# Kernel tuning notes

Hardware: AMD Instinct MI355X
Metric: run time of the kernel (lower is better)

Reference implementation:

```python
import jax, jax.numpy as jnp
import numpy as np

N_EMBD = 512
N_EXPERTS = 4
TOP_K = 2
D_FF = 4 * N_EMBD


def setup_inputs() -> dict:
    key = jax.random.key(0)
    k_x, k_g, k_w1, k_w2 = jax.random.split(key, 4)
    b, t = 8, 2048
    x = jax.random.normal(k_x, (b, t, N_EMBD), dtype=jnp.float32)
    # Linear layers are bias-free; kaiming-uniform-ish init scale
    gate_w = jax.random.normal(k_g, (N_EMBD, N_EXPERTS), dtype=jnp.float32) * (1.0 / np.sqrt(N_EMBD))
    w1 = jax.random.normal(k_w1, (N_EXPERTS, N_EMBD, D_FF), dtype=jnp.float32) * (1.0 / np.sqrt(N_EMBD))
    w2 = jax.random.normal(k_w2, (N_EXPERTS, D_FF, N_EMBD), dtype=jnp.float32) * (1.0 / np.sqrt(D_FF))
    return {"x": x, "gate_w": gate_w, "w1": w1, "w2": w2}


def reference(x, gate_w, w1, w2):
    # Eval mode: UnitCenteredNoise and Dropout are identity.
    b, t, c = x.shape
    xf = x.reshape(b * t, c)                         # [N, C]
    n = xf.shape[0]

    gate_logits = xf @ gate_w                        # [N, E]
    gate_probs = jax.nn.softmax(gate_logits, axis=-1)
    top_w, top_i = jax.lax.top_k(gate_probs, TOP_K)  # [N, K]
    top_w = top_w / jnp.clip(jnp.sum(top_w, axis=-1, keepdims=True), 1e-6)

    # Sparse router weights [N, E]: zeros except normalized top-k probs.
    router_sparse = jnp.zeros((n, N_EXPERTS), dtype=top_w.dtype)
    router_sparse = router_sparse.at[jnp.arange(n)[:, None], top_i].set(top_w)

    # Per-expert MLP on all tokens, combined with the sparse router weights.
    # Mathematically identical to the masked dispatch/combine in the original.
    h = jnp.einsum('nc,ech->enh', xf, w1)            # [E, N, 4C]
    h = jax.nn.gelu(h, approximate=False)            # torch F.gelu default = erf
    y = jnp.einsum('enh,ehc->enc', h, w2)            # [E, N, C]
    out_flat = jnp.einsum('ne,enc->nc', router_sparse, y)

    return out_flat.reshape(b, t, c), router_sparse
```

## Files before the change

kernel.cpp:

```cpp
#include <hip/hip_runtime.h>
#include <hip/hip_fp16.h>


#define NTOK  16384
#define CDIM  512
#define FF    2048
#define NEXP  4
#define CAP   33280
#define NBLK  260
#define BM    128
#define BN1   128
#define BN2   128
#define BK    32
#define CPAD  32

typedef _Float16 f16;
typedef __attribute__((ext_vector_type(8))) _Float16 f16x8;
typedef __attribute__((ext_vector_type(4))) _Float16 f16x4;
typedef __attribute__((ext_vector_type(4))) float f32x4;

__device__ __forceinline__ void gload16(const void* g, void* l) {
  __builtin_amdgcn_global_load_lds(
      (const __attribute__((address_space(1))) unsigned int*)g,
      (__attribute__((address_space(3))) unsigned int*)l, 16, 0, 0);
}

__device__ __forceinline__ float gelu_fast(float v) {
  float az = fabsf(v) * 0.7071067811865476f;
  float t = __builtin_amdgcn_rcpf(fmaf(0.3275911f, az, 1.0f));
  float p = fmaf(fmaf(fmaf(fmaf(1.061405429f, t, -1.453152027f), t,
                           1.421413741f), t, -0.284496736f), t, 0.254829592f) * t;
  float e = __builtin_amdgcn_exp2f(az * az * -1.4426950408889634f);
  float erfa = fmaf(-p, e, 1.0f);
  float u = copysignf(erfa, v);
  return 0.5f * v * (1.0f + u);
}

__device__ __forceinline__ int xcd_swz(int bid, int nwg) {
  int q = nwg >> 3, r = nwg & 7;
  int x = bid & 7, o = bid >> 3;
  return (x < r ? x * (q + 1) : r * (q + 1) + (x - r) * q) + o;
}


__global__ __launch_bounds__(256) void k_init(int* list, int* cnt) {
  int i = blockIdx.x * 256 + threadIdx.x;
  if (i < CAP) list[i] = -1;
  if (i < 4) cnt[i * CPAD] = 0;
}

__global__ __launch_bounds__(256) void k_cast_t(const float* __restrict__ in,
                                                f16* __restrict__ out, int R, int Cc) {
  __shared__ f16 T[64][72];
  int ez = blockIdx.z;
  const float* ine = in + (size_t)ez * R * Cc;
  f16* oute = out + (size_t)ez * R * Cc;
  int c0 = blockIdx.x * 64;
  int r0 = blockIdx.y * 64;
  int t = threadIdx.x;
  {
    int rr = t >> 2, cc = (t & 3) * 16;
    const float* src = ine + (size_t)(r0 + rr) * Cc + c0 + cc;
    union { f16 h[16]; uint4 u[2]; } pk;
#pragma unroll
    for (int j = 0; j < 16; j += 4) {
      float4 a = *(const float4*)(src + j);
      pk.h[j] = (f16)a.x; pk.h[j + 1] = (f16)a.y;
      pk.h[j + 2] = (f16)a.z; pk.h[j + 3] = (f16)a.w;
    }
    *(uint4*)&T[rr][cc] = pk.u[0];
    *(uint4*)&T[rr][cc + 8] = pk.u[1];
  }
  __syncthreads();
  {
    int oc = t >> 2, orr = (t & 3) * 16;
    union { f16 h[16]; uint4 u[2]; } pk;
#pragma unroll
    for (int j = 0; j < 16; ++j) pk.h[j] = T[orr + j][oc];
    f16* dst = oute + (size_t)(c0 + oc) * R + r0 + orr;
    *(uint4*)dst = pk.u[0];
    *(uint4*)(dst + 8) = pk.u[1];
  }
}


__global__ __launch_bounds__(256) void k_router(const float* __restrict__ x,
                                                const float* __restrict__ gw,
                                                f16* __restrict__ xh,
                                                float* __restrict__ rout,
                                                float4* __restrict__ tokinfo,
                                                int* __restrict__ cnt) {
  __shared__ int lcnt[4];
  int tid = threadIdx.x;
  if (tid < 4) lcnt[tid] = 0;
  __syncthreads();
  int wv = tid >> 6, lane = tid & 63;
  const float4* g = ((const float4*)gw) + lane * 8;
  float4 gv[8];
#pragma unroll
  for (int j = 0; j < 8; ++j) gv[j] = g[j];

  int tok0 = blockIdx.x * 64 + wv * 16;
  for (int i = 0; i < 16; ++i) {
    int tok = tok0 + i;
    const float4* xr = (const float4*)(x + (size_t)tok * CDIM + lane * 8);
    float4 a0 = xr[0], a1 = xr[1];
    union { f16 h[8]; uint4 u; } pk;
    pk.h[0] = (f16)a0.x; pk.h[1] = (f16)a0.y; pk.h[2] = (f16)a0.z; pk.h[3] = (f16)a0.w;
    pk.h[4] = (f16)a1.x; pk.h[5] = (f16)a1.y; pk.h[6] = (f16)a1.z; pk.h[7] = (f16)a1.w;
    *(uint4*)(xh + (size_t)tok * CDIM + lane * 8) = pk.u;
    float xv[8] = {a0.x, a0.y, a0.z, a0.w, a1.x, a1.y, a1.z, a1.w};
    float l0 = 0, l1 = 0, l2 = 0, l3 = 0;
#pragma unroll
    for (int j = 0; j < 8; ++j) {
      float4 g4 = gv[j];
      l0 = fmaf(xv[j], g4.x, l0); l1 = fmaf(xv[j], g4.y, l1);
      l2 = fmaf(xv[j], g4.z, l2); l3 = fmaf(xv[j], g4.w, l3);
    }
#pragma unroll
    for (int off = 32; off; off >>= 1) {
      l0 += __shfl_xor(l0, off); l1 += __shfl_xor(l1, off);
      l2 += __shfl_xor(l2, off); l3 += __shfl_xor(l3, off);
    }
    if (lane == 0) {
      float lg[4] = {l0, l1, l2, l3};
      float m = fmaxf(fmaxf(lg[0], lg[1]), fmaxf(lg[2], lg[3]));
      float p[4], s = 0.f;
#pragma unroll
      for (int e = 0; e < 4; ++e) { p[e] = expf(lg[e] - m); s += p[e]; }
      int i0 = 0;
#pragma unroll
      for (int e = 1; e < 4; ++e) if (lg[e] > lg[i0]) i0 = e;
      int i1 = -1;
#pragma unroll
      for (int e = 0; e < 4; ++e)
        if (e != i0 && (i1 < 0 || lg[e] > lg[i1])) i1 = e;
      float p0 = p[i0] / s, p1 = p[i1] / s;
      float ss = fmaxf(p0 + p1, 1e-6f);
      float w0 = p0 / ss, w1v = p1 / ss;
      float r[4] = {0.f, 0.f, 0.f, 0.f};
      r[i0] = w0; r[i1] = w1v;
      *(float4*)(rout + tok * 4) = make_float4(r[0], r[1], r[2], r[3]);
      float4 ti;
      ti.x = __int_as_float(i0); ti.y = __int_as_float(i1); ti.z = w0; ti.w = w1v;
      tokinfo[tok] = ti;
      atomicAdd(&lcnt[i0], 1);
      atomicAdd(&lcnt[i1], 1);
    }
  }
  __syncthreads();
  if (tid < 4) atomicAdd(cnt + tid * CPAD, lcnt[tid]);
}

__global__ void k_bases(const int* __restrict__ cnt, int* __restrict__ base,
                        int* __restrict__ cursor) {
  if (threadIdx.x == 0 && blockIdx.x == 0) {
    int b = 0;
#pragma unroll
    for (int e = 0; e < 4; ++e) {
      base[e] = b; cursor[e * CPAD] = b;
      b += (cnt[e * CPAD] + 127) & ~127;
    }
    base[4] = b;
  }
}

__global__ __launch_bounds__(256) void k_assign(const float4* __restrict__ tokinfo,
                                                int* cursor, int* __restrict__ list,
                                                int2* __restrict__ tokslot) {
  __shared__ int lcnt[4], lbase[4];
  int tid = threadIdx.x;
  if (tid < 4) lcnt[tid] = 0;
  __syncthreads();
  int t0 = blockIdx.x * 1024 + tid * 4;
  float4 ti[4]; int lo0[4], lo1[4];
#pragma unroll
  for (int j = 0; j < 4; ++j) {
    ti[j] = tokinfo[t0 + j];
    lo0[j] = atomicAdd(&lcnt[__float_as_int(ti[j].x)], 1);
    lo1[j] = atomicAdd(&lcnt[__float_as_int(ti[j].y)], 1);
  }
  __syncthreads();
  if (tid < 4) lbase[tid] = atomicAdd(cursor + tid * CPAD, lcnt[tid]);
  __syncthreads();
#pragma unroll
  for (int j = 0; j < 4; ++j) {
    int s0 = lbase[__float_as_int(ti[j].x)] + lo0[j];
    list[s0] = t0 + j;
    int s1 = lbase[__float_as_int(ti[j].y)] + lo1[j];
    list[s1] = t0 + j;
    tokslot[t0 + j] = make_int2(s0, s1);
  }
}


__global__ __launch_bounds__(256, 4) void k_gemm1(const f16* __restrict__ xh,
                                                  const f16* __restrict__ w1t,
                                                  const int* __restrict__ list,
                                                  const int* __restrict__ base,
                                                  f16* __restrict__ H, int cb, int nwg) {
  __shared__ __align__(16) char smem[32768 + 512];
  int* slist = (int*)(smem + 32768);
  int tid = threadIdx.x;
  int wk = xcd_swz(blockIdx.x, nwg);
  int bx = wk >> 4, by = wk & 15;
  int m0 = (cb + bx) * BM;
  int mloc = bx * BM;
  int h0 = by * BN1;
  int e = 0;
#pragma unroll
  for (int i = 1; i < 4; ++i) if (m0 >= base[i]) e = i;
  if (tid < BM) {
    int v = list[m0 + tid];
    slist[tid] = v < 0 ? 0 : v;
  }
  __syncthreads();

  int tokr[2];
#pragma unroll
  for (int i = 0; i < 2; ++i) tokr[i] = slist[i * 64 + (tid >> 2)];

  const f16* wB = w1t + (size_t)(e * FF + h0) * CDIM;
  int kbs = ((tid & 3) * 16) ^ (((tid >> 3) & 3) << 4);

  f32x4 acc[4][4] = {};
  int lane = tid & 63, w = tid >> 6, wr = w >> 1, wc = w & 1;

  auto stage = [&](int kk, int p) {
    char* s = smem + p * 16384;
#pragma unroll
    for (int i = 0; i < 2; ++i) {
      gload16(xh + (size_t)tokr[i] * CDIM + kk * BK + (kbs >> 1),
              s + i * 4096 + tid * 16);
    }
#pragma unroll
    for (int i = 0; i < 2; ++i) {
      int row = i * 64 + (tid >> 2);
      gload16(wB + (size_t)row * CDIM + kk * BK + (kbs >> 1),
              s + 8192 + i * 4096 + tid * 16);
    }
  };

  auto compute = [&](int p) {
    const char* s = smem + p * 16384;
    f16x8 af[4], bfr[4];
    int kb = (lane >> 4) * 16;
#pragma unroll
    for (int fr = 0; fr < 4; ++fr) {
      int row = wr * 64 + fr * 16 + (lane & 15);
      af[fr] = *(const f16x8*)(s + row * 64 + (kb ^ (((row >> 1) & 3) << 4)));
    }
#pragma unroll
    for (int fc = 0; fc < 4; ++fc) {
      int col = wc * 64 + fc * 16 + (lane & 15);
      bfr[fc] = *(const f16x8*)(s + 8192 + col * 64 + (kb ^ (((col >> 1) & 3) << 4)));
    }
#pragma unroll
    for (int fr = 0; fr < 4; ++fr)
#pragma unroll
      for (int fc = 0; fc < 4; ++fc)
        acc[fr][fc] = __builtin_amdgcn_mfma_f32_16x16x32_f16(af[fr], bfr[fc],
                                                             acc[fr][fc], 0, 0, 0);
  };

  stage(0, 0);
  __syncthreads();
  for (int kk = 0; kk < 16; ++kk) {
    if (kk < 15) stage(kk + 1, (kk + 1) & 1);
    __builtin_amdgcn_sched_barrier(0);
    __builtin_amdgcn_s_setprio(1);
    compute(kk & 1);
    __builtin_amdgcn_s_setprio(0);
    __syncthreads();
  }

#pragma unroll
  for (int fr = 0; fr < 4; ++fr)
#pragma unroll
    for (int fc = 0; fc < 4; ++fc)
#pragma unroll
      for (int i = 0; i < 4; ++i) {
        int row = wr * 64 + fr * 16 + (lane >> 4) * 4 + i;
        int col = wc * 64 + fc * 16 + (lane & 15);
        float v = gelu_fast(acc[fr][fc][i]);
        int off = (row * 256 + col * 2) ^ ((row & 7) << 4);
        *(f16*)(smem + off) = (f16)v;
      }
  __syncthreads();
#pragma unroll
  for (int j = 0; j < 8; ++j) {
    int row = j * 16 + (tid >> 4);
    int colb = ((tid & 15) * 16) ^ ((row & 7) << 4);
    uint4 v = *(const uint4*)(smem + row * 256 + colb);
    *(uint4*)((char*)H + ((size_t)(mloc + row) * FF + h0) * 2 + (tid & 15) * 16) = v;
  }
}


__global__ __launch_bounds__(256, 4) void k_gemm2(const f16* __restrict__ H,
                                                  const f16* __restrict__ w2t,
                                                  const int* __restrict__ base,
                                                  f16* __restrict__ Y, int cb, int nwg) {
  __shared__ __align__(16) char smem[32768];
  int tid = threadIdx.x;
  int wk = xcd_swz(blockIdx.x, nwg);
  int bx = wk >> 2, by = wk & 3;
  int m0 = (cb + bx) * BM;
  int mloc = bx * BM;
  int c0 = by * BN2;
  int e = 0;
#pragma unroll
  for (int i = 1; i < 4; ++i) if (m0 >= base[i]) e = i;

  const f16* pA = H + (size_t)mloc * FF;
  const f16* wB = w2t + (size_t)(e * CDIM + c0) * FF;
  int kbs = ((tid & 3) * 16) ^ (((tid >> 3) & 3) << 4);

  f32x4 acc[4][4] = {};
  int lane = tid & 63, w = tid >> 6, wr = w >> 1, wc = w & 1;

  auto stage = [&](int kk, int p) {
    char* s = smem + p * 16384;
#pragma unroll
    for (int i = 0; i < 2; ++i) {
      int row = i * 64 + (tid >> 2);
      gload16(pA + (size_t)row * FF + kk * BK + (kbs >> 1),
              s + i * 4096 + tid * 16);
    }
#pragma unroll
    for (int i = 0; i < 2; ++i) {
      int row = i * 64 + (tid >> 2);
      gload16(wB + (size_t)row * FF + kk * BK + (kbs >> 1),
              s + 8192 + i * 4096 + tid * 16);
    }
  };

  auto compute = [&](int p) {
    const char* s = smem + p * 16384;
    f16x8 af[4], bfr[4];
    int kb = (lane >> 4) * 16;
#pragma unroll
    for (int fr = 0; fr < 4; ++fr) {
      int row = wr * 64 + fr * 16 + (lane & 15);
      af[fr] = *(const f16x8*)(s + row * 64 + (kb ^ (((row >> 1) & 3) << 4)));
    }
#pragma unroll
    for (int fc = 0; fc < 4; ++fc) {
      int col = wc * 64 + fc * 16 + (lane & 15);
      bfr[fc] = *(const f16x8*)(s + 8192 + col * 64 + (kb ^ (((col >> 1) & 3) << 4)));
    }
#pragma unroll
    for (int fr = 0; fr < 4; ++fr)
#pragma unroll
      for (int fc = 0; fc < 4; ++fc)
        acc[fr][fc] = __builtin_amdgcn_mfma_f32_16x16x32_f16(af[fr], bfr[fc],
                                                             acc[fr][fc], 0, 0, 0);
  };

  stage(0, 0);
  __syncthreads();
  for (int kk = 0; kk < 64; ++kk) {
    if (kk < 63) stage(kk + 1, (kk + 1) & 1);
    __builtin_amdgcn_sched_barrier(0);
    __builtin_amdgcn_s_setprio(1);
    compute(kk & 1);
    __builtin_amdgcn_s_setprio(0);
    __syncthreads();
  }

#pragma unroll
  for (int fr = 0; fr < 4; ++fr)
#pragma unroll
    for (int fc = 0; fc < 4; ++fc)
#pragma unroll
      for (int i = 0; i < 4; ++i) {
        int row = wr * 64 + fr * 16 + (lane >> 4) * 4 + i;
        int col = wc * 64 + fc * 16 + (lane & 15);
        int off = (row * 256 + col * 2) ^ ((row & 7) << 4);
        *(f16*)(smem + off) = (f16)acc[fr][fc][i];
      }
  __syncthreads();
#pragma unroll
  for (int j = 0; j < 8; ++j) {
    int row = j * 16 + (tid >> 4);
    int colb = ((tid & 15) * 16) ^ ((row & 7) << 4);
    uint4 v = *(const uint4*)(smem + row * 256 + colb);
    *(uint4*)((char*)Y + ((size_t)(m0 + row) * CDIM + c0) * 2 + (tid & 15) * 16) = v;
  }
}


__global__ __launch_bounds__(256) void k_combine(const f16* __restrict__ Y,
                                                 const float4* __restrict__ tokinfo,
                                                 const int2* __restrict__ tokslot,
                                                 float* __restrict__ out) {
  int gid = blockIdx.x * 256 + threadIdx.x;
  int tok = gid >> 7;
  int cc = (gid & 127) * 4;
  int2 sl = tokslot[tok];
  float4 ti = tokinfo[tok];
  f16x4 y0 = *(const f16x4*)(Y + (size_t)sl.x * CDIM + cc);
  f16x4 y1 = *(const f16x4*)(Y + (size_t)sl.y * CDIM + cc);
  float w0 = ti.z, w1 = ti.w;
  float4 o;
  o.x = w0 * (float)y0[0] + w1 * (float)y1[0];
  o.y = w0 * (float)y0[1] + w1 * (float)y1[1];
  o.z = w0 * (float)y0[2] + w1 * (float)y1[2];
  o.w = w0 * (float)y0[3] + w1 * (float)y1[3];
  *(float4*)(out + (size_t)tok * CDIM + cc) = o;
}


extern "C" void kernel_launch(void* const* d_in, const int* in_sizes, int n_in,
                              void* d_out, int out_size, void* d_ws, size_t ws_size,
                              hipStream_t stream) {
  const float* x  = (const float*)d_in[0];
  const float* gw = (const float*)d_in[1];
  const float* w1 = (const float*)d_in[2];
  const float* w2 = (const float*)d_in[3];
  float* out  = (float*)d_out;
  float* rout = out + (size_t)NTOK * CDIM;

  char* ws = (char*)d_ws;
  f16* xh      = (f16*)ws;      ws += (size_t)NTOK * CDIM * 2;
  f16* w1t     = (f16*)ws;      ws += (size_t)NEXP * FF * CDIM * 2;
  f16* w2t     = (f16*)ws;      ws += (size_t)NEXP * FF * CDIM * 2;
  f16* Ybuf    = (f16*)ws;      ws += (size_t)CAP * CDIM * 2;
  float4* tokinfo = (float4*)ws; ws += (size_t)NTOK * 16;
  int2* tokslot = (int2*)ws;    ws += (size_t)NTOK * 8;
  int* list    = (int*)ws;      ws += (size_t)CAP * 4;
  int* cnt     = (int*)ws;      ws += 4 * CPAD * 4;
  int* base    = (int*)ws;      ws += 64;
  int* cursor  = (int*)ws;      ws += 4 * CPAD * 4;
  f16* Hbuf    = (f16*)ws;

  size_t base_bytes = (size_t)(ws - (char*)d_ws);
  const int opts[12] = {260, 130, 65, 52, 26, 20, 13, 10, 5, 4, 2, 1};
  int CB = 1;
  for (int oi = 0; oi < 12; ++oi) {
    if (base_bytes + (size_t)opts[oi] * BM * FF * 2 <= ws_size) { CB = opts[oi]; break; }
  }

  k_init<<<(CAP + 255) / 256, 256, 0, stream>>>(list, cnt);
  k_cast_t<<<dim3(FF / 64, CDIM / 64, NEXP), 256, 0, stream>>>(w1, w1t, CDIM, FF);
  k_cast_t<<<dim3(CDIM / 64, FF / 64, NEXP), 256, 0, stream>>>(w2, w2t, FF, CDIM);
  k_router<<<NTOK / 64, 256, 0, stream>>>(x, gw, xh, rout, tokinfo, cnt);
  k_bases<<<1, 64, 0, stream>>>(cnt, base, cursor);
  k_assign<<<NTOK / 1024, 256, 0, stream>>>(tokinfo, cursor, list, tokslot);

  for (int cb = 0; cb < NBLK; cb += CB) {
    int n1 = CB * 16, n2 = CB * 4;
    k_gemm1<<<n1, 256, 0, stream>>>(xh, w1t, list, base, Hbuf, cb, n1);
    k_gemm2<<<n2, 256, 0, stream>>>(Hbuf, w2t, base, Ybuf, cb, n2);
  }
  k_combine<<<NTOK * CDIM / 4 / 256, 256, 0, stream>>>(Ybuf, tokinfo, tokslot, out);
}
```

Baseline: 264.5 us.

## Use 256-row tiles with 512 threads and a triple-buffered A pipeline

Both expert GEMMs now use 512-thread blocks covering 256 token rows each, so every staged weight tile is shared across twice as many rows. Expert segments are padded to 256 rows to match. The A operand is triple-buffered and B double-buffered, with explicit vmcnt waits so the next loads are issued before the MFMAs and only one barrier runs per k-step. The larger blocks use 64KB of LDS each, which cuts how many blocks fit per CU, and the extra padding adds some wasted rows.

Result: slower. 286.1 us (+8.2%).

```diff
diff --git a/kernel.cpp b/kernel.cpp
--- a/kernel.cpp
+++ b/kernel.cpp
@@ -6,12 +6,11 @@
 #define CDIM  512
 #define FF    2048
 #define NEXP  4
-#define CAP   33280
-#define NBLK  260
+#define CAP   33792
+#define NBLK  264
 #define BM    128
-#define BN1   128
-#define BN2   128
-#define BK    32
+#define NT1   16
+#define NT2   64
 #define CPAD  32
 
 typedef _Float16 f16;
@@ -159,7 +158,7 @@
 #pragma unroll
     for (int e = 0; e < 4; ++e) {
       base[e] = b; cursor[e * CPAD] = b;
-      b += (cnt[e * CPAD] + 127) & ~127;
+      b += (cnt[e * CPAD] + 255) & ~255;
     }
     base[4] = b;
   }
@@ -194,23 +193,23 @@
 }
 
 
-__global__ __launch_bounds__(256, 4) void k_gemm1(const f16* __restrict__ xh,
+__global__ __launch_bounds__(512, 4) void k_gemm1(const f16* __restrict__ xh,
                                                   const f16* __restrict__ w1t,
                                                   const int* __restrict__ list,
                                                   const int* __restrict__ base,
                                                   f16* __restrict__ H, int cb, int nwg) {
-  __shared__ __align__(16) char smem[32768 + 512];
-  int* slist = (int*)(smem + 32768);
+  __shared__ __align__(16) char smem[66560];
+  int* slist = (int*)(smem + 65536);
   int tid = threadIdx.x;
   int wk = xcd_swz(blockIdx.x, nwg);
   int bx = wk >> 4, by = wk & 15;
-  int m0 = (cb + bx) * BM;
-  int mloc = bx * BM;
-  int h0 = by * BN1;
+  int m0 = cb * BM + bx * 256;
+  int mloc = bx * 256;
+  int h0 = by * 128;
   int e = 0;
 #pragma unroll
   for (int i = 1; i < 4; ++i) if (m0 >= base[i]) e = i;
-  if (tid < BM) {
+  if (tid < 256) {
     int v = list[m0 + tid];
     slist[tid] = v < 0 ? 0 : v;
   }
@@ -218,7 +217,7 @@
 
   int tokr[2];
 #pragma unroll
-  for (int i = 0; i < 2; ++i) tokr[i] = slist[i * 64 + (tid >> 2)];
+  for (int l = 0; l < 2; ++l) tokr[l] = slist[l * 128 + (tid >> 2)];
 
   const f16* wB = w1t + (size_t)(e * FF + h0) * CDIM;
   int kbs = ((tid & 3) * 16) ^ (((tid >> 3) & 3) << 4);
@@ -226,52 +225,57 @@
   f32x4 acc[4][4] = {};
   int lane = tid & 63, w = tid >> 6, wr = w >> 1, wc = w & 1;
 
-  auto stage = [&](int kk, int p) {
-    char* s = smem + p * 16384;
-#pragma unroll
-    for (int i = 0; i < 2; ++i) {
-      gload16(xh + (size_t)tokr[i] * CDIM + kk * BK + (kbs >> 1),
-              s + i * 4096 + tid * 16);
-    }
-#pragma unroll
-    for (int i = 0; i < 2; ++i) {
-      int row = i * 64 + (tid >> 2);
-      gload16(wB + (size_t)row * CDIM + kk * BK + (kbs >> 1),
-              s + 8192 + i * 4096 + tid * 16);
-    }
+  auto stageA = [&](int kt) {
+    char* s = smem + (kt % 3) * 16384;
+#pragma unroll
+    for (int l = 0; l < 2; ++l)
+      gload16(xh + (size_t)tokr[l] * CDIM + kt * 32 + (kbs >> 1),
+              s + l * 8192 + tid * 16);
   };
-
-  auto compute = [&](int p) {
-    const char* s = smem + p * 16384;
-    f16x8 af[4], bfr[4];
+  auto stageB = [&](int kt) {
+    char* s = smem + 49152 + (kt & 1) * 8192;
+    gload16(wB + (size_t)(tid >> 2) * CDIM + kt * 32 + (kbs >> 1), s + tid * 16);
+  };
+
+  for (int kt = 0; kt < 2; ++kt) stageA(kt);
+  stageB(0);
+  asm volatile("s_waitcnt vmcnt(0)" ::: "memory");
+  __builtin_amdgcn_s_barrier();
+
+  for (int t = 0; t < NT1; ++t) {
+    const char* sA = smem + (t % 3) * 16384;
+    const char* sB = smem + 49152 + (t & 1) * 8192;
     int kb = (lane >> 4) * 16;
+    f16x8 af[4], bf[4];
+#pragma unroll
+    for (int fc = 0; fc < 4; ++fc) {
+      int col = wc * 64 + fc * 16 + (lane & 15);
+      bf[fc] = *(const f16x8*)(sB + col * 64 + (kb ^ (((col >> 1) & 3) << 4)));
+    }
 #pragma unroll
     for (int fr = 0; fr < 4; ++fr) {
       int row = wr * 64 + fr * 16 + (lane & 15);
-      af[fr] = *(const f16x8*)(s + row * 64 + (kb ^ (((row >> 1) & 3) << 4)));
-    }
-#pragma unroll
-    for (int fc = 0; fc < 4; ++fc) {
-      int col = wc * 64 + fc * 16 + (lane & 15);
-      bfr[fc] = *(const f16x8*)(s + 8192 + col * 64 + (kb ^ (((col >> 1) & 3) << 4)));
-    }
-#pragma unroll
-    for (int fr = 0; fr < 4; ++fr)
-#pragma unroll
-      for (int fc = 0; fc < 4; ++fc)
-        acc[fr][fc] = __builtin_amdgcn_mfma_f32_16x16x32_f16(af[fr], bfr[fc],
-                                                             acc[fr][fc], 0, 0, 0);
-  };
-
-  stage(0, 0);
-  __syncthreads();
-  for (int kk = 0; kk < 16; ++kk) {
-    if (kk < 15) stage(kk + 1, (kk + 1) & 1);
+      af[fr] = *(const f16x8*)(sA + row * 64 + (kb ^ (((row >> 1) & 3) << 4)));
+    }
+    if (t + 1 < NT1) stageB(t + 1);
+    if (t + 2 < NT1) {
+      stageA(t + 2);
+      asm volatile("s_waitcnt vmcnt(2)" ::: "memory");
+    } else {
+      asm volatile("s_waitcnt vmcnt(0)" ::: "memory");
+    }
+    asm volatile("s_waitcnt lgkmcnt(0)" ::: "memory");
     __builtin_amdgcn_sched_barrier(0);
     __builtin_amdgcn_s_setprio(1);
-    compute(kk & 1);
+#pragma unroll
+    for (int fr = 0; fr < 4; ++fr)
+#pragma unroll
+      for (int fc = 0; fc < 4; ++fc)
+        acc[fr][fc] = __builtin_amdgcn_mfma_f32_16x16x32_f16(af[fr], bf[fc],
+                                                             acc[fr][fc], 0, 0, 0);
     __builtin_amdgcn_s_setprio(0);
-    __syncthreads();
+    __builtin_amdgcn_sched_barrier(0);
+    __builtin_amdgcn_s_barrier();
   }
 
 #pragma unroll
@@ -289,7 +293,7 @@
   __syncthreads();
 #pragma unroll
   for (int j = 0; j < 8; ++j) {
-    int row = j * 16 + (tid >> 4);
+    int row = j * 32 + (tid >> 4);
     int colb = ((tid & 15) * 16) ^ ((row & 7) << 4);
     uint4 v = *(const uint4*)(smem + row * 256 + colb);
     *(uint4*)((char*)H + ((size_t)(mloc + row) * FF + h0) * 2 + (tid & 15) * 16) = v;
@@ -297,17 +301,17 @@
 }
 
 
-__global__ __launch_bounds__(256, 4) void k_gemm2(const f16* __restrict__ H,
+__global__ __launch_bounds__(512, 4) void k_gemm2(const f16* __restrict__ H,
                                                   const f16* __restrict__ w2t,
                                                   const int* __restrict__ base,
                                                   f16* __restrict__ Y, int cb, int nwg) {
-  __shared__ __align__(16) char smem[32768];
+  __shared__ __align__(16) char smem[65536];
   int tid = threadIdx.x;
   int wk = xcd_swz(blockIdx.x, nwg);
   int bx = wk >> 2, by = wk & 3;
-  int m0 = (cb + bx) * BM;
-  int mloc = bx * BM;
-  int c0 = by * BN2;
+  int m0 = cb * BM + bx * 256;
+  int mloc = bx * 256;
+  int c0 = by * 128;
   int e = 0;
 #pragma unroll
   for (int i = 1; i < 4; ++i) if (m0 >= base[i]) e = i;
@@ -319,53 +323,58 @@
   f32x4 acc[4][4] = {};
   int lane = tid & 63, w = tid >> 6, wr = w >> 1, wc = w & 1;
 
-  auto stage = [&](int kk, int p) {
-    char* s = smem + p * 16384;
-#pragma unroll
-    for (int i = 0; i < 2; ++i) {
-      int row = i * 64 + (tid >> 2);
-      gload16(pA + (size_t)row * FF + kk * BK + (kbs >> 1),
-              s + i * 4096 + tid * 16);
-    }
-#pragma unroll
-    for (int i = 0; i < 2; ++i) {
-      int row = i * 64 + (tid >> 2);
-      gload16(wB + (size_t)row * FF + kk * BK + (kbs >> 1),
-              s + 8192 + i * 4096 + tid * 16);
+  auto stageA = [&](int kt) {
+    char* s = smem + (kt % 3) * 16384;
+#pragma unroll
+    for (int l = 0; l < 2; ++l) {
+      int row = l * 128 + (tid >> 2);
+      gload16(pA + (size_t)row * FF + kt * 32 + (kbs >> 1), s + l * 8192 + tid * 16);
     }
   };
-
-  auto compute = [&](int p) {
-    const char* s = smem + p * 16384;
-    f16x8 af[4], bfr[4];
+  auto stageB = [&](int kt) {
+    char* s = smem + 49152 + (kt & 1) * 8192;
+    gload16(wB + (size_t)(tid >> 2) * FF + kt * 32 + (kbs >> 1), s + tid * 16);
+  };
+
+  for (int kt = 0; kt < 2; ++kt) stageA(kt);
+  stageB(0);
+  asm volatile("s_waitcnt vmcnt(0)" ::: "memory");
+  __builtin_amdgcn_s_barrier();
+
+  for (int t = 0; t < NT2; ++t) {
+    const char* sA = smem + (t % 3) * 16384;
+    const char* sB = smem + 49152 + (t & 1) * 8192;
     int kb = (lane >> 4) * 16;
+    f16x8 af[4], bf[4];
+#pragma unroll
+    for (int fc = 0; fc < 4; ++fc) {
+      int col = wc * 64 + fc * 16 + (lane & 15);
+      bf[fc] = *(const f16x8*)(sB + col * 64 + (kb ^ (((col >> 1) & 3) << 4)));
+    }
 #pragma unroll
     for (int fr = 0; fr < 4; ++fr) {
       int row = wr * 64 + fr * 16 + (lane & 15);
-      af[fr] = *(const f16x8*)(s + row * 64 + (kb ^ (((row >> 1) & 3) << 4)));
-    }
-#pragma unroll
-    for (int fc = 0; fc < 4; ++fc) {
-      int col = wc * 64 + fc * 16 + (lane & 15);
-      bfr[fc] = *(const f16x8*)(s + 8192 + col * 64 + (kb ^ (((col >> 1) & 3) << 4)));
-    }
-#pragma unroll
-    for (int fr = 0; fr < 4; ++fr)
-#pragma unroll
-      for (int fc = 0; fc < 4; ++fc)
-        acc[fr][fc] = __builtin_amdgcn_mfma_f32_16x16x32_f16(af[fr], bfr[fc],
-                                                             acc[fr][fc], 0, 0, 0);
-  };
-
-  stage(0, 0);
-  __syncthreads();
-  for (int kk = 0; kk < 64; ++kk) {
-    if (kk < 63) stage(kk + 1, (kk + 1) & 1);
+      af[fr] = *(const f16x8*)(sA + row * 64 + (kb ^ (((row >> 1) & 3) << 4)));
+    }
+    if (t + 1 < NT2) stageB(t + 1);
+    if (t + 2 < NT2) {
+      stageA(t + 2);
+      asm volatile("s_waitcnt vmcnt(2)" ::: "memory");
+    } else {
+      asm volatile("s_waitcnt vmcnt(0)" ::: "memory");
+    }
+    asm volatile("s_waitcnt lgkmcnt(0)" ::: "memory");
     __builtin_amdgcn_sched_barrier(0);
     __builtin_amdgcn_s_setprio(1);
-    compute(kk & 1);
+#pragma unroll
+    for (int fr = 0; fr < 4; ++fr)
+#pragma unroll
+      for (int fc = 0; fc < 4; ++fc)
+        acc[fr][fc] = __builtin_amdgcn_mfma_f32_16x16x32_f16(af[fr], bf[fc],
+                                                             acc[fr][fc], 0, 0, 0);
     __builtin_amdgcn_s_setprio(0);
-    __syncthreads();
+    __builtin_amdgcn_sched_barrier(0);
+    __builtin_amdgcn_s_barrier();
   }
 
 #pragma unroll
@@ -382,7 +391,7 @@
   __syncthreads();
 #pragma unroll
   for (int j = 0; j < 8; ++j) {
-    int row = j * 16 + (tid >> 4);
+    int row = j * 32 + (tid >> 4);
     int colb = ((tid & 15) * 16) ^ ((row & 7) << 4);
     uint4 v = *(const uint4*)(smem + row * 256 + colb);
     *(uint4*)((char*)Y + ((size_t)(m0 + row) * CDIM + c0) * 2 + (tid & 15) * 16) = v;
@@ -435,9 +444,9 @@
   f16* Hbuf    = (f16*)ws;
 
   size_t base_bytes = (size_t)(ws - (char*)d_ws);
-  const int opts[12] = {260, 130, 65, 52, 26, 20, 13, 10, 5, 4, 2, 1};
-  int CB = 1;
-  for (int oi = 0; oi < 12; ++oi) {
+  const int opts[9] = {264, 132, 88, 44, 22, 12, 8, 4, 2};
+  int CB = 2;
+  for (int oi = 0; oi < 9; ++oi) {
     if (base_bytes + (size_t)opts[oi] * BM * FF * 2 <= ws_size) { CB = opts[oi]; break; }
   }
 
@@ -449,9 +458,9 @@
   k_assign<<<NTOK / 1024, 256, 0, stream>>>(tokinfo, cursor, list, tokslot);
 
   for (int cb = 0; cb < NBLK; cb += CB) {
-    int n1 = CB * 16, n2 = CB * 4;
-    k_gemm1<<<n1, 256, 0, stream>>>(xh, w1t, list, base, Hbuf, cb, n1);
-    k_gemm2<<<n2, 256, 0, stream>>>(Hbuf, w2t, base, Ybuf, cb, n2);
+    int n1 = (CB / 2) * 16, n2 = (CB / 2) * 4;
+    k_gemm1<<<n1, 512, 0, stream>>>(xh, w1t, list, base, Hbuf, cb, n1);
+    k_gemm2<<<n2, 512, 0, stream>>>(Hbuf, w2t, base, Ybuf, cb, n2);
   }
   k_combine<<<NTOK * CDIM / 4 / 256, 256, 0, stream>>>(Ybuf, tokinfo, tokslot, out);
 }
```

## Add 256x256-tile second GEMM with 512 threads and triple-buffered LDS

Applied to the files above, without the earlier changes.

Adds a new down-projection kernel that computes 256x256 output tiles with 8 waves, a three-stage LDS ring fed by direct global-to-LDS loads, split A/B staging interleaved with MFMA phases, and raised wave priority during MFMA. Expert segments are padded to 256 rows so each tile stays within one expert, which raises capacity and block count. The new path is used only when the workspace holds the whole H buffer; otherwise the old chunked loop runs. The router also uses four times as many blocks with fewer tokens each. Larger tiles reduce redundant global loads of H and W2 but increase padding waste and LDS use per block, which limits occupancy.

Result: slower. 282.8 us (+6.9%).

```diff
diff --git a/kernel.cpp b/kernel.cpp
--- a/kernel.cpp
+++ b/kernel.cpp
@@ -6,12 +6,12 @@
 #define CDIM  512
 #define FF    2048
 #define NEXP  4
-#define CAP   33280
-#define NBLK  260
+#define CAP   33792
+#define NBLK  264
 #define BM    128
 #define BN1   128
-#define BN2   128
 #define BK    32
+#define NT2   64
 #define CPAD  32
 
 typedef _Float16 f16;
@@ -100,8 +100,8 @@
 #pragma unroll
   for (int j = 0; j < 8; ++j) gv[j] = g[j];
 
-  int tok0 = blockIdx.x * 64 + wv * 16;
-  for (int i = 0; i < 16; ++i) {
+  int tok0 = blockIdx.x * 16 + wv * 4;
+  for (int i = 0; i < 4; ++i) {
     int tok = tok0 + i;
     const float4* xr = (const float4*)(x + (size_t)tok * CDIM + lane * 8);
     float4 a0 = xr[0], a1 = xr[1];
@@ -159,7 +159,7 @@
 #pragma unroll
     for (int e = 0; e < 4; ++e) {
       base[e] = b; cursor[e * CPAD] = b;
-      b += (cnt[e * CPAD] + 127) & ~127;
+      b += (cnt[e * CPAD] + 255) & ~255;
     }
     base[4] = b;
   }
@@ -297,6 +297,131 @@
 }
 
 
+__global__ __launch_bounds__(512, 2) void k_gemm2r(const f16* __restrict__ H,
+                                                   const f16* __restrict__ w2t,
+                                                   const int* __restrict__ base,
+                                                   f16* __restrict__ Y, int nwg) {
+  __shared__ __align__(16) char smem[131072];
+  int tid = threadIdx.x;
+  int wk = xcd_swz(blockIdx.x, nwg);
+  int bx = wk >> 1, by = wk & 1;
+  int m0 = bx * 256;
+  int c0 = by * 256;
+  int e = 0;
+#pragma unroll
+  for (int i = 1; i < 4; ++i) if (m0 >= base[i]) e = i;
+
+  const f16* pA = H + (size_t)m0 * FF;
+  const f16* wB = w2t + (size_t)(e * CDIM + c0) * FF;
+  int kbs = ((tid & 3) * 16) ^ (((tid >> 3) & 3) << 4);
+
+  f32x4 acc[8][4] = {};
+  int lane = tid & 63, w = tid >> 6, wr = w >> 2, wc = w & 3;
+
+  int kb = (lane >> 4) * 16;
+  int aoff[8], boff[4];
+#pragma unroll
+  for (int fr = 0; fr < 8; ++fr) {
+    int row = wr * 128 + fr * 16 + (lane & 15);
+    aoff[fr] = row * 64 + (kb ^ (((row >> 1) & 3) << 4));
+  }
+#pragma unroll
+  for (int fc = 0; fc < 4; ++fc) {
+    int col = wc * 64 + fc * 16 + (lane & 15);
+    boff[fc] = 16384 + col * 64 + (kb ^ (((col >> 1) & 3) << 4));
+  }
+
+  auto stageA = [&](int kt, int sb) {
+    char* s = smem + sb;
+#pragma unroll
+    for (int l = 0; l < 2; ++l) {
+      int row = l * 128 + (tid >> 2);
+      gload16(pA + (size_t)row * FF + kt * BK + (kbs >> 1), s + l * 8192 + tid * 16);
+    }
+  };
+  auto stageB = [&](int kt, int sb) {
+    char* s = smem + sb + 16384;
+#pragma unroll
+    for (int l = 0; l < 2; ++l) {
+      int row = l * 128 + (tid >> 2);
+      gload16(wB + (size_t)row * FF + kt * BK + (kbs >> 1), s + l * 8192 + tid * 16);
+    }
+  };
+
+  stageA(0, 0); stageB(0, 0);
+  stageA(1, 32768); stageB(1, 32768);
+  asm volatile("s_waitcnt vmcnt(4)" ::: "memory");
+  __builtin_amdgcn_s_barrier();
+
+  int scur = 0, sst = 65536;
+  f16x8 af[4], bf[4];
+  for (int kt = 0; kt < NT2; ++kt) {
+    const char* s = smem + scur;
+#pragma unroll
+    for (int fc = 0; fc < 4; ++fc) bf[fc] = *(const f16x8*)(s + boff[fc]);
+#pragma unroll
+    for (int fr = 0; fr < 4; ++fr) af[fr] = *(const f16x8*)(s + aoff[fr]);
+    if (kt < NT2 - 2) stageA(kt + 2, sst);
+    __builtin_amdgcn_s_barrier();
+    asm volatile("s_waitcnt lgkmcnt(0)" ::: "memory");
+    __builtin_amdgcn_sched_barrier(0);
+    __builtin_amdgcn_s_setprio(1);
+#pragma unroll
+    for (int fr = 0; fr < 4; ++fr)
+#pragma unroll
+      for (int fc = 0; fc < 4; ++fc)
+        acc[fr][fc] = __builtin_amdgcn_mfma_f32_16x16x32_f16(af[fr], bf[fc],
+                                                             acc[fr][fc], 0, 0, 0);
+    __builtin_amdgcn_s_setprio(0);
+    __builtin_amdgcn_sched_barrier(0);
+    __builtin_amdgcn_s_barrier();
+#pragma unroll
+    for (int fr = 0; fr < 4; ++fr) af[fr] = *(const f16x8*)(s + aoff[4 + fr]);
+    if (kt < NT2 - 2) {
+      stageB(kt + 2, sst);
+      asm volatile("s_waitcnt vmcnt(4)" ::: "memory");
+    } else {
+      asm volatile("s_waitcnt vmcnt(0)" ::: "memory");
+    }
+    __builtin_amdgcn_s_barrier();
+    asm volatile("s_waitcnt lgkmcnt(0)" ::: "memory");
+    __builtin_amdgcn_sched_barrier(0);
+    __builtin_amdgcn_s_setprio(1);
+#pragma unroll
+    for (int fr = 0; fr < 4; ++fr)
+#pragma unroll
+      for (int fc = 0; fc < 4; ++fc)
+        acc[4 + fr][fc] = __builtin_amdgcn_mfma_f32_16x16x32_f16(af[fr], bf[fc],
+                                                                 acc[4 + fr][fc], 0, 0, 0);
+    __builtin_amdgcn_s_setprio(0);
+    __builtin_amdgcn_sched_barrier(0);
+    __builtin_amdgcn_s_barrier();
+    scur = (scur == 65536) ? 0 : scur + 32768;
+    sst  = (sst  == 65536) ? 0 : sst  + 32768;
+  }
+
+#pragma unroll
+  for (int fr = 0; fr < 8; ++fr)
+#pragma unroll
+    for (int fc = 0; fc < 4; ++fc)
+#pragma unroll
+      for (int i = 0; i < 4; ++i) {
+        int row = wr * 128 + fr * 16 + (lane >> 4) * 4 + i;
+        int col = wc * 64 + fc * 16 + (lane & 15);
+        int off = row * 512 + ((col * 2) ^ ((row & 7) << 4));
+        *(f16*)(smem + off) = (f16)acc[fr][fc][i];
+      }
+  __syncthreads();
+#pragma unroll
+  for (int j = 0; j < 16; ++j) {
+    int row = j * 16 + (tid >> 5);
+    int colb = ((tid & 31) * 16) ^ ((row & 7) << 4);
+    uint4 v = *(const uint4*)(smem + row * 512 + colb);
+    *(uint4*)((char*)Y + ((size_t)(m0 + row) * CDIM + c0) * 2 + (tid & 31) * 16) = v;
+  }
+}
+
+
 __global__ __launch_bounds__(256, 4) void k_gemm2(const f16* __restrict__ H,
                                                   const f16* __restrict__ w2t,
                                                   const int* __restrict__ base,
@@ -307,7 +432,7 @@
   int bx = wk >> 2, by = wk & 3;
   int m0 = (cb + bx) * BM;
   int mloc = bx * BM;
-  int c0 = by * BN2;
+  int c0 = by * 128;
   int e = 0;
 #pragma unroll
   for (int i = 1; i < 4; ++i) if (m0 >= base[i]) e = i;
@@ -435,23 +560,30 @@
   f16* Hbuf    = (f16*)ws;
 
   size_t base_bytes = (size_t)(ws - (char*)d_ws);
-  const int opts[12] = {260, 130, 65, 52, 26, 20, 13, 10, 5, 4, 2, 1};
-  int CB = 1;
-  for (int oi = 0; oi < 12; ++oi) {
+  const int opts[9] = {264, 132, 88, 44, 22, 12, 8, 4, 2};
+  int CB = 2;
+  for (int oi = 0; oi < 9; ++oi) {
     if (base_bytes + (size_t)opts[oi] * BM * FF * 2 <= ws_size) { CB = opts[oi]; break; }
   }
 
   k_init<<<(CAP + 255) / 256, 256, 0, stream>>>(list, cnt);
   k_cast_t<<<dim3(FF / 64, CDIM / 64, NEXP), 256, 0, stream>>>(w1, w1t, CDIM, FF);
   k_cast_t<<<dim3(CDIM / 64, FF / 64, NEXP), 256, 0, stream>>>(w2, w2t, FF, CDIM);
-  k_router<<<NTOK / 64, 256, 0, stream>>>(x, gw, xh, rout, tokinfo, cnt);
+  k_router<<<NTOK / 16, 256, 0, stream>>>(x, gw, xh, rout, tokinfo, cnt);
   k_bases<<<1, 64, 0, stream>>>(cnt, base, cursor);
   k_assign<<<NTOK / 1024, 256, 0, stream>>>(tokinfo, cursor, list, tokslot);
 
-  for (int cb = 0; cb < NBLK; cb += CB) {
-    int n1 = CB * 16, n2 = CB * 4;
-    k_gemm1<<<n1, 256, 0, stream>>>(xh, w1t, list, base, Hbuf, cb, n1);
-    k_gemm2<<<n2, 256, 0, stream>>>(Hbuf, w2t, base, Ybuf, cb, n2);
+  if (CB == NBLK) {
+    int n1 = NBLK * 16;
+    k_gemm1<<<n1, 256, 0, stream>>>(xh, w1t, list, base, Hbuf, 0, n1);
+    int n2 = (NBLK / 2) * 2;
+    k_gemm2r<<<n2, 512, 0, stream>>>(Hbuf, w2t, base, Ybuf, n2);
+  } else {
+    for (int cb = 0; cb < NBLK; cb += CB) {
+      int n1 = CB * 16, n2 = CB * 4;
+      k_gemm1<<<n1, 256, 0, stream>>>(xh, w1t, list, base, Hbuf, cb, n1);
+      k_gemm2<<<n2, 256, 0, stream>>>(Hbuf, w2t, base, Ybuf, cb, n2);
+    }
   }
   k_combine<<<NTOK * CDIM / 4 / 256, 256, 0, stream>>>(Ybuf, tokinfo, tokslot, out);
 }
```
